# Kernel tuning notes

Hardware: AMD Instinct MI355X
Metric: run time of the kernel (lower is better)

Reference implementation:

```python
import jax, jax.numpy as jnp
import numpy as np

N_NODES = 8192
D = 7      # in_dim == out_dim (hardcoded 7x7 weight)
K = 32     # kNN fan-out


def setup_inputs() -> dict:
    key = jax.random.key(0)
    k1, k2, k3 = jax.random.split(key, 3)
    x = jax.random.normal(k1, (N_NODES, D + 1), dtype=jnp.float32)
    W = jax.random.normal(k2, (D, D), dtype=jnp.float32) * np.float32(1.0 / np.sqrt(D))
    a = jax.random.normal(k3, (2 * D,), dtype=jnp.float32) * np.float32(0.1)
    return {"x": x, "W": W, "a": a}


def _forward(x, W, a, k=K):
    # split pollutant channel (last column) from features, as in the torch forward
    pollutant = x[:, -1]          # (N,)
    feat = x[:, :-1]              # (N, D)
    N, d = feat.shape

    # linear transform (nn.functional.linear(x, weight) == x @ W.T)
    out = feat @ W.T              # (N, D)
    # nonlinearity_1 = Hardtanh
    out = jnp.clip(out, -1.0, 1.0)
    # (feature_weight = softmax(a) is computed in torch but unused for 'affine' kernel)

    # kNN graph built from input features (use_previous_graph=True).
    # Squared distances give the same neighbor ordering as euclidean norms.
    sq = jnp.sum(feat * feat, axis=1)                       # (N,)
    dist2 = sq[:, None] + sq[None, :] - 2.0 * (feat @ feat.T)
    dist2 = jnp.maximum(dist2, 0.0)
    dist2 = jnp.where(jnp.eye(N, dtype=bool), jnp.inf, dist2)  # dist[dist==0] = inf (self)
    _, nbr = jax.lax.top_k(-dist2, k)                       # (N, k) nearest neighbors

    out_n = out[nbr]                                        # (N, k, D) neighbor gather
    # affine attention: score_ij = concat(out_i, out_j) . a
    s = (out @ a[:d])[:, None] + out_n @ a[d:]              # (N, k)
    att = jax.nn.softmax(s, axis=-1)                        # per-node softmax over neighbors

    pol_n = pollutant[nbr]                                  # (N, k)
    xp = jnp.concatenate([out_n, pol_n[..., None]], axis=-1)  # (N, k, D+1)
    agg = jnp.einsum('nk,nkd->nd', att, xp)                 # attention-weighted aggregate

    y = jnp.concatenate([out, agg], axis=-1)                # (N, 2D+1)
    return y, att


def reference(x, W, a):
    y, att = _forward(x, W, a)
    # torch returns (y, y_, a) where y_ is y and a is the last node's attention row
    return (y, y, att[-1])
```

## Files before the change

kernel.cpp:

```cpp
#include <hip/hip_runtime.h>
#include <math.h>
#include <stdint.h>

#define N_NODES 8192
#define D 7
#define K 32
#define NT 512
#define QB 16
#define CPT (N_NODES / NT)
#define TPW 64
#define SCAP 320
#define ECAP2 256
#define DELTA 0.125f

typedef unsigned long long u64;
typedef _Float16 h2 __attribute__((ext_vector_type(2)));
typedef _Float16 f16x8 __attribute__((ext_vector_type(8)));
typedef float f32x4 __attribute__((ext_vector_type(4)));
union U4H8 { uint4 u; f16x8 h; };

__device__ __forceinline__ unsigned pkh(float a, float b) {
    union { h2 h; unsigned u; } t;
    t.h[0] = (_Float16)a; t.h[1] = (_Float16)b; return t.u;
}
__device__ __forceinline__ unsigned ordu(float f) {
    unsigned u = __float_as_uint(f);
    return (u & 0x80000000u) ? ~u : (u | 0x80000000u);
}
__device__ __forceinline__ float unordu(unsigned o) {
    unsigned u = (o & 0x80000000u) ? (o & 0x7fffffffu) : ~o;
    return __uint_as_float(u);
}

__device__ __forceinline__ float dist_m(float4 b0, float4 b1, float sqj,
                                        float4 A, float4 B) {
    float dot = A.x * b0.x;
    dot = fmaf(A.y, b0.y, dot);
    dot = fmaf(A.z, b0.z, dot);
    dot = fmaf(A.w, b0.w, dot);
    dot = fmaf(B.x, b1.x, dot);
    dot = fmaf(B.y, b1.y, dot);
    dot = fmaf(B.z, b1.z, dot);
    return fmaf(-2.0f, dot, sqj);
}

__global__ __launch_bounds__(256)
void precompute_kernel(const float* __restrict__ x, const float* __restrict__ W,
                       float* __restrict__ outb, uint4* __restrict__ fh,
                       float4* __restrict__ xsq4)
{
    int n = blockIdx.x * 256 + threadIdx.x;
    float4 v0 = *reinterpret_cast<const float4*>(x + n * 8);
    float4 v1 = *reinterpret_cast<const float4*>(x + n * 8 + 4);
    float f[D] = {v0.x, v0.y, v0.z, v0.w, v1.x, v1.y, v1.z};
    float sq = 0.f;
#pragma unroll
    for (int c = 0; c < D; ++c) sq += f[c] * f[c];
    uint4 h;
    h.x = pkh(f[0], f[1]); h.y = pkh(f[2], f[3]);
    h.z = pkh(f[4], f[5]); h.w = pkh(f[6], sq);
    fh[n] = h;
    xsq4[n * 2]     = v0;
    xsq4[n * 2 + 1] = make_float4(v1.x, v1.y, v1.z, sq);
#pragma unroll
    for (int r = 0; r < D; ++r) {
        float acc = 0.f;
#pragma unroll
        for (int c = 0; c < D; ++c) acc += f[c] * W[r * D + c];
        acc = fminf(fmaxf(acc, -1.f), 1.f);
        outb[n * D + r] = acc;
    }
}

__global__ __launch_bounds__(NT, 2)
void gat_kernel(const float* __restrict__ x, const float* __restrict__ aw,
                const float* __restrict__ outb, const uint4* __restrict__ fh,
                const float4* __restrict__ xs4, float* __restrict__ dout)
{
    __shared__ u64      cand[QB][ECAP2];
    __shared__ unsigned short ent[QB][SCAP];
    __shared__ int      nbr[QB][K];
    __shared__ uint4    qpk[QB];
    __shared__ float4   qf4[QB][2];
    __shared__ float    sqfL[QB];
    __shared__ unsigned selT[QB];
    __shared__ float    exqL[QB];
    __shared__ float    scrL[QB];
    __shared__ int      scnt[QB];
    __shared__ int      cnt2[QB];
    __shared__ float    redv[8];
    __shared__ int      redi[8];
    __shared__ float    bcv;
    __shared__ int      bci;

    float* Lmin = (float*)cand;

    const int tid  = threadIdx.x;
    const int lane = tid & 63;
    const int wave = tid >> 6;
    const int i0   = blockIdx.x * QB;
    const int col  = lane & 15;
    const int lg   = lane >> 4;

    if (tid < QB) {
        float4 b0 = xs4[(i0 + tid) * 2];
        float4 b1 = xs4[(i0 + tid) * 2 + 1];
        qpk[tid] = make_uint4(pkh(-2.f * b0.x, -2.f * b0.y),
                              pkh(-2.f * b0.z, -2.f * b0.w),
                              pkh(-2.f * b1.x, -2.f * b1.y),
                              pkh(-2.f * b1.z, 1.0f));
        qf4[tid][0] = b0;
        qf4[tid][1] = b1;
        sqfL[tid]   = b1.w;
        scnt[tid] = 0;
        cnt2[tid] = 0;
    }
    __syncthreads();

    U4H8 ub; ub.u = (lane < QB) ? qpk[lane] : make_uint4(0u, 0u, 0u, 0u);
    const f16x8 bfrag = ub.h;
    const f32x4 z4 = {0.f, 0.f, 0.f, 0.f};
    const int tb = wave * TPW;

    float lm0 = INFINITY, lm1 = INFINITY, lm2 = INFINITY, lm3 = INFINITY;
#pragma unroll 4
    for (int tt = 0; tt < TPW / 2; ++tt) {
        int t = tb + tt;
        uint4 au = make_uint4(0u, 0u, 0u, 0u);
        if (lane < 16) au = fh[t * 16 + lane];
        U4H8 ua; ua.u = au;
        f32x4 acc = __builtin_amdgcn_mfma_f32_16x16x32_f16(ua.h, bfrag, z4, 0, 0, 0);
        lm0 = fminf(lm0, acc[0]);
        lm1 = fminf(lm1, acc[1]);
        lm2 = fminf(lm2, acc[2]);
        lm3 = fminf(lm3, acc[3]);
    }
    {
        int sb = wave * 16 + lg * 4;
        Lmin[(sb + 0) * 16 + col] = lm0;
        Lmin[(sb + 1) * 16 + col] = lm1;
        Lmin[(sb + 2) * 16 + col] = lm2;
        Lmin[(sb + 3) * 16 + col] = lm3;
    }
    __syncthreads();

#pragma unroll
    for (int h = 0; h < 2; ++h) {
        const int q = wave + h * 8;
        unsigned ov0 = ordu(Lmin[lane * 16 + q]);
        unsigned ov1 = ordu(Lmin[(64 + lane) * 16 + q]);
        unsigned lo = 0u, hi = 0xFFFFFFFFu;
        while (lo < hi) {
            unsigned mid = lo + ((hi - lo) >> 1);
            int cnt = __popcll(__ballot(ov0 <= mid))
                    + __popcll(__ballot(ov1 <= mid));
            if (cnt >= 34) hi = mid; else lo = mid + 1;
        }
        if (lane == 0) selT[q] = lo;
    }
    __syncthreads();

    if (tid < QB) {
        float Ts  = unordu(selT[tid]);
        float sq_ = sqfL[tid];
        exqL[tid] = fmaxf(Ts + DELTA, -sq_);
        scrL[tid] = fmaxf(Ts + 2.f * DELTA, -sq_ + DELTA);
    }
    __syncthreads();

    {
        float myscr = scrL[col];
#pragma unroll 4
        for (int tt = 0; tt < TPW; ++tt) {
            int t = tb + tt;
            uint4 au = make_uint4(0u, 0u, 0u, 0u);
            if (lane < 16) au = fh[t * 16 + lane];
            U4H8 ua; ua.u = au;
            f32x4 acc = __builtin_amdgcn_mfma_f32_16x16x32_f16(ua.h, bfrag, z4, 0, 0, 0);
            float v01 = fminf(acc[0], acc[1]);
            float v23 = fminf(acc[2], acc[3]);
            if (fminf(v01, v23) <= myscr) {
#pragma unroll
                for (int r = 0; r < 4; ++r) {
                    if (acc[r] <= myscr) {
                        int j = t * 16 + lg * 4 + r;
                        int p = atomicAdd(&scnt[col], 1);
                        if (p < SCAP) ent[col][p] = (unsigned short)j;
                    }
                }
            }
        }
    }
    __syncthreads();

#pragma unroll 1
    for (int q = 0; q < QB; ++q) {
        int n = scnt[q];
        if (n > SCAP) n = SCAP;
        float4 A  = qf4[q][0];
        float4 Bv = qf4[q][1];
        float thr = exqL[q];
        for (int t = tid; t < n; t += NT) {
            int j = ent[q][t];
            float4 b0 = xs4[j * 2];
            float4 b1 = xs4[j * 2 + 1];
            float m = dist_m(b0, b1, b1.w, A, Bv);
            if (m <= thr && j != i0 + q) {
                float d2c = fmaxf(Bv.w + m, 0.f);
                u64 key = ((u64)__float_as_uint(d2c) << 32) | (unsigned)j;
                int p = atomicAdd(&cnt2[q], 1);
                if (p < ECAP2) cand[q][p] = key;
            }
        }
    }
    __syncthreads();

#pragma unroll
    for (int h = 0; h < 2; ++h) {
        const int q = wave + h * 8;
        const int M = cnt2[q];
        if (scnt[q] <= SCAP && M >= K && M <= ECAP2) {
            for (int p = lane; p < M; p += 64) {
                u64 my = cand[q][p];
                int rank = 0;
                for (int m = 0; m < M; ++m)
                    rank += (cand[q][m] < my) ? 1 : 0;
                if (rank < K) nbr[q][rank] = (int)(my & 0xffffffffu);
            }
        }
    }
    __syncthreads();

#pragma unroll 1
    for (int q = 0; q < QB; ++q) {
        int s = scnt[q];
        int M = cnt2[q];
        if (s > SCAP || M < K || M > ECAP2) {
            const int iq = i0 + q;
            float4 A  = qf4[q][0];
            float4 Bv = qf4[q][1];
            float lastv = -1.0f; int lasti = -1;
#pragma unroll 1
            for (int it = 0; it < K; ++it) {
                float best = INFINITY; int bidx = 0x7fffffff;
#pragma unroll 1
                for (int c = 0; c < CPT; ++c) {
                    int j = c * NT + tid;
                    float4 b0 = xs4[j * 2];
                    float4 b1 = xs4[j * 2 + 1];
                    float m = dist_m(b0, b1, b1.w, A, Bv);
                    float d2c = fmaxf(Bv.w + m, 0.f);
                    if (j == iq) continue;
                    bool gt = (d2c > lastv) || (d2c == lastv && j > lasti);
                    if (gt && (d2c < best || (d2c == best && j < bidx))) {
                        best = d2c; bidx = j;
                    }
                }
#pragma unroll
                for (int off = 32; off > 0; off >>= 1) {
                    float ov = __shfl_down(best, off);
                    int   oi = __shfl_down(bidx, off);
                    if (ov < best || (ov == best && oi < bidx)) { best = ov; bidx = oi; }
                }
                if (lane == 0) { redv[wave] = best; redi[wave] = bidx; }
                __syncthreads();
                if (tid == 0) {
                    float bv = redv[0]; int bi = redi[0];
#pragma unroll
                    for (int w = 1; w < 8; ++w)
                        if (redv[w] < bv || (redv[w] == bv && redi[w] < bi)) {
                            bv = redv[w]; bi = redi[w];
                        }
                    bcv = bv; bci = bi;
                    nbr[q][it] = bi;
                }
                __syncthreads();
                lastv = bcv; lasti = bci;
            }
        }
    }
    __syncthreads();

#pragma unroll 1
    for (int h = 0; h < 2; ++h) {
        const int q  = wave + h * 8;
        const int iq = i0 + q;
        if (lane < K) {
            int nk = nbr[q][lane];
            float s = 0.f;
#pragma unroll
            for (int c = 0; c < D; ++c) s += outb[iq * D + c] * aw[c];
            float xp[D + 1];
#pragma unroll
            for (int c = 0; c < D; ++c) {
                float on = outb[nk * D + c];
                xp[c] = on;
                s += on * aw[D + c];
            }
            xp[D] = x[nk * 8 + 7];

            float m = s;
#pragma unroll
            for (int off = 16; off > 0; off >>= 1) m = fmaxf(m, __shfl_xor(m, off, 32));
            float e = expf(s - m);
            float sum = e;
#pragma unroll
            for (int off = 16; off > 0; off >>= 1) sum += __shfl_xor(sum, off, 32);
            float att = e / sum;

            float agg[D + 1];
#pragma unroll
            for (int dd = 0; dd < D + 1; ++dd) {
                float v = att * xp[dd];
#pragma unroll
                for (int off = 16; off > 0; off >>= 1) v += __shfl_xor(v, off, 32);
                agg[dd] = v;
            }

            if (lane < D) {
                float o = outb[iq * D + lane];
                dout[iq * 15 + lane] = o;
                dout[N_NODES * 15 + iq * 15 + lane] = o;
            }
            if (lane < D + 1) {
                float av_ = agg[0];
#pragma unroll
                for (int dd = 1; dd < D + 1; ++dd) av_ = (lane == dd) ? agg[dd] : av_;
                dout[iq * 15 + D + lane] = av_;
                dout[N_NODES * 15 + iq * 15 + D + lane] = av_;
            }
            if (iq == N_NODES - 1) dout[2 * N_NODES * 15 + lane] = att;
        }
    }
}

extern "C" void kernel_launch(void* const* d_in, const int* in_sizes, int n_in,
                              void* d_out, int out_size, void* d_ws, size_t ws_size,
                              hipStream_t stream) {
    (void)in_sizes; (void)n_in; (void)out_size; (void)ws_size;
    const float* x = (const float*)d_in[0];
    const float* W = (const float*)d_in[1];
    const float* a = (const float*)d_in[2];
    float* out   = (float*)d_out;
    float* outb  = (float*)d_ws;
    uint4* fh    = (uint4*)(outb + N_NODES * D);
    float4* xsq4 = (float4*)(fh + N_NODES);

    hipLaunchKernelGGL(precompute_kernel, dim3(N_NODES / 256), dim3(256),
                       0, stream, x, W, outb, fh, xsq4);
    hipLaunchKernelGGL(gat_kernel, dim3(N_NODES / QB), dim3(NT),
                       0, stream, x, a, outb, fh, xsq4, out);
}
```

Baseline: 73.64 us.

## Replace iterative argmin fallback with radix-style bisection select; enlarge candidate caps

The slow fallback for queries whose candidate lists overflowed ran K sequential block-wide argmin passes over all nodes. It is replaced by a bisection over packed 64-bit (distance, index) keys held in registers, which finds the 33rd-smallest key threshold and then feeds the exact-rank stage. The candidate refinement loop now gives each wave its own query instead of having the whole block sweep every query serially. SCAP and ECAP2 are raised so fewer queries overflow, at the cost of more shared memory (which may reduce occupancy) and up to 64 barrier-bound bisection iterations per fallback query.

New measurement: 109.5 us. +48.7%, slower.

```diff
diff --git a/kernel.cpp b/kernel.cpp
--- a/kernel.cpp
+++ b/kernel.cpp
@@ -9,8 +9,8 @@
 #define QB 16
 #define CPT (N_NODES / NT)
 #define TPW 64
-#define SCAP 320
-#define ECAP2 256
+#define SCAP 512
+#define ECAP2 384
 #define DELTA 0.125f
 
 typedef unsigned long long u64;
@@ -88,10 +88,7 @@
     __shared__ float    scrL[QB];
     __shared__ int      scnt[QB];
     __shared__ int      cnt2[QB];
-    __shared__ float    redv[8];
-    __shared__ int      redi[8];
-    __shared__ float    bcv;
-    __shared__ int      bci;
+    __shared__ int      cntR;
 
     float* Lmin = (float*)cand;
 
@@ -193,14 +190,15 @@
     }
     __syncthreads();
 
-#pragma unroll 1
-    for (int q = 0; q < QB; ++q) {
+#pragma unroll
+    for (int h = 0; h < 2; ++h) {
+        const int q = wave + h * 8;
         int n = scnt[q];
         if (n > SCAP) n = SCAP;
         float4 A  = qf4[q][0];
         float4 Bv = qf4[q][1];
         float thr = exqL[q];
-        for (int t = tid; t < n; t += NT) {
+        for (int t = lane; t < n; t += 64) {
             int j = ent[q][t];
             float4 b0 = xs4[j * 2];
             float4 b1 = xs4[j * 2 + 1];
@@ -215,67 +213,66 @@
     }
     __syncthreads();
 
+#pragma unroll 1
+    for (int q = 0; q < QB; ++q) {
+        int s = scnt[q];
+        int M = cnt2[q];
+        if (s <= SCAP && M >= K && M <= ECAP2) continue;
+        const int iq = i0 + q;
+        float4 A  = qf4[q][0];
+        float4 Bv = qf4[q][1];
+        u64 kr[CPT];
+#pragma unroll
+        for (int c = 0; c < CPT; ++c) {
+            int j = c * NT + tid;
+            float4 b0 = xs4[j * 2];
+            float4 b1 = xs4[j * 2 + 1];
+            float m = dist_m(b0, b1, b1.w, A, Bv);
+            float d2c = fmaxf(Bv.w + m, 0.f);
+            u64 key = ((u64)__float_as_uint(d2c) << 32) | (unsigned)j;
+            kr[c] = (j == iq) ? ~0ull : key;
+        }
+        u64 lo = 0ull, hi = ~0ull;
+#pragma unroll 1
+        while (lo < hi) {
+            u64 mid = lo + ((hi - lo) >> 1);
+            int lc = 0;
+#pragma unroll
+            for (int c = 0; c < CPT; ++c) lc += (kr[c] <= mid) ? 1 : 0;
+#pragma unroll
+            for (int off = 32; off > 0; off >>= 1) lc += __shfl_down(lc, off);
+            if (tid == 0) cntR = 0;
+            __syncthreads();
+            if (lane == 0) atomicAdd(&cntR, lc);
+            __syncthreads();
+            int tot = cntR;
+            if (tot >= 33) hi = mid; else lo = mid + 1;
+            __syncthreads();
+        }
+        if (tid == 0) cnt2[q] = 0;
+        __syncthreads();
+#pragma unroll
+        for (int c = 0; c < CPT; ++c) {
+            if (kr[c] <= lo) {
+                int p = atomicAdd(&cnt2[q], 1);
+                if (p < ECAP2) cand[q][p] = kr[c];
+            }
+        }
+        if (tid < QB && tid == q) scnt[q] = 0;
+        __syncthreads();
+    }
+
 #pragma unroll
     for (int h = 0; h < 2; ++h) {
         const int q = wave + h * 8;
         const int M = cnt2[q];
-        if (scnt[q] <= SCAP && M >= K && M <= ECAP2) {
+        if (M >= K && M <= ECAP2) {
             for (int p = lane; p < M; p += 64) {
                 u64 my = cand[q][p];
                 int rank = 0;
                 for (int m = 0; m < M; ++m)
                     rank += (cand[q][m] < my) ? 1 : 0;
                 if (rank < K) nbr[q][rank] = (int)(my & 0xffffffffu);
-            }
-        }
-    }
-    __syncthreads();
-
-#pragma unroll 1
-    for (int q = 0; q < QB; ++q) {
-        int s = scnt[q];
-        int M = cnt2[q];
-        if (s > SCAP || M < K || M > ECAP2) {
-            const int iq = i0 + q;
-            float4 A  = qf4[q][0];
-            float4 Bv = qf4[q][1];
-            float lastv = -1.0f; int lasti = -1;
-#pragma unroll 1
-            for (int it = 0; it < K; ++it) {
-                float best = INFINITY; int bidx = 0x7fffffff;
-#pragma unroll 1
-                for (int c = 0; c < CPT; ++c) {
-                    int j = c * NT + tid;
-                    float4 b0 = xs4[j * 2];
-                    float4 b1 = xs4[j * 2 + 1];
-                    float m = dist_m(b0, b1, b1.w, A, Bv);
-                    float d2c = fmaxf(Bv.w + m, 0.f);
-                    if (j == iq) continue;
-                    bool gt = (d2c > lastv) || (d2c == lastv && j > lasti);
-                    if (gt && (d2c < best || (d2c == best && j < bidx))) {
-                        best = d2c; bidx = j;
-                    }
-                }
-#pragma unroll
-                for (int off = 32; off > 0; off >>= 1) {
-                    float ov = __shfl_down(best, off);
-                    int   oi = __shfl_down(bidx, off);
-                    if (ov < best || (ov == best && oi < bidx)) { best = ov; bidx = oi; }
-                }
-                if (lane == 0) { redv[wave] = best; redi[wave] = bidx; }
-                __syncthreads();
-                if (tid == 0) {
-                    float bv = redv[0]; int bi = redi[0];
-#pragma unroll
-                    for (int w = 1; w < 8; ++w)
-                        if (redv[w] < bv || (redv[w] == bv && redi[w] < bi)) {
-                            bv = redv[w]; bi = redi[w];
-                        }
-                    bcv = bv; bci = bi;
-                    nbr[q][it] = bi;
-                }
-                __syncthreads();
-                lastv = bcv; lasti = bci;
             }
         }
     }
```
